# Optimization experiments

Hardware: AMD Instinct MI355X
Metric: run time of the kernel (lower is better)

The kernel has to match this reference:

```python
import jax, jax.numpy as jnp
import numpy as np

N = 50000      # total atoms/beads across batch
E = 800000     # total edges (avg degree 16)
H = 128        # hidden_channels
R = 50         # num_rbf
NB = 2         # n_interaction blocks
NG = 64        # num graphs in batch
NT = 100       # num atom types
CUT = 5.0      # upper distance cutoff


def setup_inputs() -> dict:
    key = jax.random.key(0)
    ks = jax.random.split(key, 20)
    atom_types = jax.random.randint(ks[0], (N,), 0, NT)
    pos = jax.random.uniform(ks[1], (N, 3), jnp.float32) * 30.0  # box of 30 Angstrom
    edge_index = jax.random.randint(ks[2], (2, E), 0, N)
    batch = jnp.sort(jax.random.randint(ks[3], (N,), 0, NG))

    def g(k, shape, fan_in):
        return jax.random.normal(k, shape, jnp.float32) * (1.0 / fan_in) ** 0.5

    emb = jax.random.normal(ks[4], (NT, H), jnp.float32) * 0.1
    # filter network per block: Linear(R->H) -> tanh -> Linear(H->H)
    fw1 = g(ks[5], (NB, R, H), R)
    fb1 = jnp.zeros((NB, H), jnp.float32)
    fw2 = g(ks[6], (NB, H, H), H)
    fb2 = jnp.zeros((NB, H), jnp.float32)
    # CFConv lin1 (no bias), lin2 (bias)
    lin1_w = g(ks[7], (NB, H, H), H)
    lin2_w = g(ks[8], (NB, H, H), H)
    lin2_b = jnp.zeros((NB, H), jnp.float32)
    # InteractionBlock output linear
    blk_w = g(ks[9], (NB, H, H), H)
    blk_b = jnp.zeros((NB, H), jnp.float32)
    # output network: Linear(H->H/2) -> tanh -> Linear(H/2->1)
    out_w1 = g(ks[10], (H, H // 2), H)
    out_b1 = jnp.zeros((H // 2,), jnp.float32)
    out_w2 = g(ks[11], (H // 2, 1), H // 2)
    out_b2 = jnp.zeros((1,), jnp.float32)
    return dict(atom_types=atom_types, pos=pos, edge_index=edge_index, batch=batch,
                emb=emb, fw1=fw1, fb1=fb1, fw2=fw2, fb2=fb2,
                lin1_w=lin1_w, lin2_w=lin2_w, lin2_b=lin2_b,
                blk_w=blk_w, blk_b=blk_b,
                out_w1=out_w1, out_b1=out_b1, out_w2=out_w2, out_b2=out_b2)


def reference(atom_types, pos, edge_index, batch, emb, fw1, fb1, fw2, fb2,
              lin1_w, lin2_w, lin2_b, blk_w, blk_b,
              out_w1, out_b1, out_w2, out_b2):
    src, dst = edge_index[0], edge_index[1]
    # pairwise distances along edges (eps keeps sqrt grad finite at coincident points)
    diff = pos[src] - pos[dst]                                  # [E,3]
    d = jnp.sqrt(jnp.sum(diff * diff, axis=-1) + 1e-12)         # [E]
    # Gaussian RBF expansion
    offsets = jnp.linspace(0.0, CUT, R)
    coeff = -0.5 / (offsets[1] - offsets[0]) ** 2
    rbf = jnp.exp(coeff * (d[:, None] - offsets) ** 2)          # [E,R]
    # cosine cutoff envelope
    Cenv = jnp.where(d < CUT, 0.5 * (jnp.cos(d * jnp.pi / CUT) + 1.0), 0.0)  # [E]

    x = emb[atom_types]                                          # [N,H]
    for i in range(NB):
        # filter generation from expanded distances
        W = jnp.tanh(rbf @ fw1[i] + fb1[i]) @ fw2[i] + fb2[i]    # [E,H]
        W = W * Cenv[:, None]
        # CFConv: lin1 -> gather*filter -> scatter-sum -> lin2
        h = x @ lin1_w[i]                                        # [N,H]
        msg = h[src] * W                                         # [E,H]
        agg = jax.ops.segment_sum(msg, dst, num_segments=N)      # [N,H]
        h = agg @ lin2_w[i] + lin2_b[i]
        # InteractionBlock: activation -> lin, residual add in SchNet.forward
        h = jnp.tanh(h)
        x = x + (h @ blk_w[i] + blk_b[i])
    # output network -> per-atom energy, scatter-sum per graph
    e = jnp.tanh(x @ out_w1 + out_b1) @ out_w2 + out_b2          # [N,1]
    energy = jax.ops.segment_sum(e, batch, num_segments=NG)      # [NG,1]
    return energy.flatten()
```

## Files before the change

kernel.cpp:

```cpp
#include <hip/hip_runtime.h>
#include <hip/hip_bf16.h>
#include <math.h>

#define H 128
#define RBF 50
#define CUTF 5.0f
#define PIF 3.14159265358979323846f
#define QT 1024
#define DEGC 16

__global__ __launch_bounds__(256) void prep_kernel(
    const float* __restrict__ pos, float4* __restrict__ pos4, int Nn,
    int4* __restrict__ zbase, int zquads,
    const float* __restrict__ fw1, const float* __restrict__ fb1,
    const float* __restrict__ fw2, const float* __restrict__ fb2,
    const float* __restrict__ lin1w, const float* __restrict__ lin2b,
    const float* __restrict__ blkw, const float* __restrict__ blkb,
    const float* __restrict__ emb,
    const float* __restrict__ ow1, const float* __restrict__ ob1,
    const float* __restrict__ ow2, const float* __restrict__ ob2,
    float* __restrict__ tab, float* __restrict__ e_type,
    float* __restrict__ htype0, float* __restrict__ htype1, int NT,
    int ZFB, int PB, int FB, int TB, int H0B)
{
// ... 105 lines not shown
        float x0 = emb[(size_t)ty * H + h0];
        float x1 = emb[(size_t)ty * H + h1];
        float a0 = 0.f, a1 = 0.f;
        #pragma unroll 8
        for (int k = 0; k < 64; ++k) {
            float bb2 = __shfl(x0, k, 64);
            a0 = fmaf(bb2, lin1w[k * H + h0], a0);
            a1 = fmaf(bb2, lin1w[k * H + h1], a1);
        }
        #pragma unroll 8
        for (int k = 0; k < 64; ++k) {
            float bb2 = __shfl(x1, k, 64);
            a0 = fmaf(bb2, lin1w[(64 + k) * H + h0], a0);
            a1 = fmaf(bb2, lin1w[(64 + k) * H + h1], a1);
        }
        htype0[(size_t)ty * H + h0] = a0;
        htype0[(size_t)ty * H + h1] = a1;
        return;
    }
    b -= H0B;
    {
        const int ty = b * 4 + (tid >> 6);
        if (ty >= NT) return;
        const float* bwp = blkw;
        float t0 = tanhf(lin2b[h0]);
        float t1 = tanhf(lin2b[h1]);
        float c0 = blkb[h0], c1 = blkb[h1];
        #pragma unroll 8
        for (int k = 0; k < 64; ++k) {
            float bb2 = __shfl(t0, k, 64);
            c0 = fmaf(bb2, bwp[k * H + h0], c0);
            c1 = fmaf(bb2, bwp[k * H + h1], c1);
        }
        #pragma unroll 8
        for (int k = 0; k < 64; ++k) {
            float bb2 = __shfl(t1, k, 64);
            c0 = fmaf(bb2, bwp[(64 + k) * H + h0], c0);
            c1 = fmaf(bb2, bwp[(64 + k) * H + h1], c1);
        }
        float x0 = emb[(size_t)ty * H + h0] + c0;
        float x1 = emb[(size_t)ty * H + h1] + c1;
        const float* l1 = lin1w + (size_t)H * H;
        float a0 = 0.f, a1 = 0.f;
        #pragma unroll 8
        for (int k = 0; k < 64; ++k) {
            float bb2 = __shfl(x0, k, 64);
            a0 = fmaf(bb2, l1[k * H + h0], a0);
            a1 = fmaf(bb2, l1[k * H + h1], a1);
        }
        #pragma unroll 8
        for (int k = 0; k < 64; ++k) {
            float bb2 = __shfl(x1, k, 64);
            a0 = fmaf(bb2, l1[(64 + k) * H + h0], a0);
            a1 = fmaf(bb2, l1[(64 + k) * H + h1], a1);
        }
        htype1[(size_t)ty * H + h0] = a0;
        htype1[(size_t)ty * H + h1] = a1;
    }
}

__global__ __launch_bounds__(256) void edge_prep_kernel(
    const float4* __restrict__ pos4, const int* __restrict__ ei, int E,
    int* __restrict__ deg, float* __restrict__ bdist, int* __restrict__ bsrc,
    int* __restrict__ is_src, int* __restrict__ is_dst)
{
    const int gtid = blockIdx.x * 256 + threadIdx.x;
    const int e0 = gtid * 4;

    int s[4], t[4];
    float d[4];
    bool act[4] = {false, false, false, false};

    if (e0 + 3 < E && (E & 3) == 0) {
        const int4 sv = *(const int4*)(ei + e0);
        const int4 tv = *(const int4*)(ei + E + e0);
        s[0] = sv.x; s[1] = sv.y; s[2] = sv.z; s[3] = sv.w;
        t[0] = tv.x; t[1] = tv.y; t[2] = tv.z; t[3] = tv.w;
        #pragma unroll
        for (int j = 0; j < 4; ++j) {
            float4 ps = pos4[s[j]], pt = pos4[t[j]];
            float dx = ps.x - pt.x, dy = ps.y - pt.y, dz = ps.z - pt.z;
            d[j] = sqrtf(dx * dx + dy * dy + dz * dz + 1e-12f);
            act[j] = (d[j] < CUTF);
        }
    } else if (e0 < E) {
        #pragma unroll
        for (int j = 0; j < 4; ++j) {
            int e = e0 + j;
            if (e < E) {
                s[j] = ei[e]; t[j] = ei[E + e];
                float4 ps = pos4[s[j]], pt = pos4[t[j]];
                float dx = ps.x - pt.x, dy = ps.y - pt.y, dz = ps.z - pt.z;
                d[j] = sqrtf(dx * dx + dy * dy + dz * dz + 1e-12f);
                act[j] = (d[j] < CUTF);
            }
        }
    }

    #pragma unroll
    for (int j = 0; j < 4; ++j) {
        if (act[j]) {
            is_src[s[j]] = 1;
            is_dst[t[j]] = 1;
            int k = atomicAdd(&deg[t[j]], 1);
            if (k < DEGC) {
                size_t bo = (size_t)t[j] * DEGC + k;
                bdist[bo] = d[j];
                bsrc[bo]  = s[j];
            }
        }
    }
}

__global__ __launch_bounds__(256) void compact_atoms_kernel(
    const int* __restrict__ is_src, const int* __restrict__ is_dst, int Nn,
    int* __restrict__ cnt4,
    int* __restrict__ dst_list, int* __restrict__ sd_list)
{
    __shared__ int wtot[2][4], wbase[2][4];
    const int tid = threadIdx.x;
    const int lane = tid & 63;
    const int wv = tid >> 6;
    int n = blockIdx.x * 256 + tid;
    bool v[2] = {false, false};
    if (n < Nn) {
        bool vd = is_dst[n] != 0;
        v[0] = vd;
        v[1] = vd && (is_src[n] != 0);
    }
    unsigned long long b[2];
    #pragma unroll
    for (int l = 0; l < 2; ++l) {
        b[l] = __ballot(v[l]);
        if (lane == 0) wtot[l][wv] = (int)__popcll(b[l]);
    }
    __syncthreads();
    if (tid == 0) {
        #pragma unroll
        for (int l = 0; l < 2; ++l) {
            int t0 = wtot[l][0], t1 = wtot[l][1], t2 = wtot[l][2], t3 = wtot[l][3];
            int tot = t0 + t1 + t2 + t3;
            int base = 0;
            if (tot) base = atomicAdd(cnt4 + 1 + l, tot);
            wbase[l][0] = base; wbase[l][1] = base + t0;
            wbase[l][2] = base + t0 + t1; wbase[l][3] = base + t0 + t1 + t2;
        }
    }
    __syncthreads();
    const unsigned long long ltm = ((unsigned long long)1 << lane) - 1;
    if (v[0]) dst_list[wbase[0][wv] + (int)__popcll(b[0] & ltm)] = n;
    if (v[1]) sd_list[wbase[1][wv] + (int)__popcll(b[1] & ltm)] = n;
}

#define STAGE_W(dstbuf, Wsrc, kcbase)                                        \
    {                                                                        \
        int wr = tid >> 5;                                                   \
        int wc = (tid & 31) * 4;                                             \
        _Pragma("unroll")                                                    \
        for (int p = 0; p < 4; ++p) {                                        \
            int row = wr + p * 8;                                            \
            *(float4*)&Ws[dstbuf][row][wc] =                                 \
                *(const float4*)((Wsrc) + (size_t)((kcbase) + row) * H + wc);\
        }                                                                    \
    }

__global__ __launch_bounds__(256) void update_x0_kernel(
    const float* __restrict__ bdist, const int* __restrict__ bsrc,
    const int* __restrict__ deg, const int* __restrict__ atype,
    const float* __restrict__ tab0, const float* __restrict__ htype0,
    const float* __restrict__ l2w, const float* __restrict__ l2b,
    const float* __restrict__ bw, const float* __restrict__ bb,
    const float* __restrict__ emb, const int* __restrict__ is_src,
    const float* __restrict__ l1w1,
    float* __restrict__ x, float* __restrict__ hbuf,
    const int* __restrict__ rows, const int* __restrict__ cntp)
{
    __shared__ float Ws[2][32][128];
    __shared__ float Tl[32][132];
    __shared__ int rlist[32], tlist[32], slist[32], dlist[32];

    const int tid = threadIdx.x;
    const int cnt = *cntp;
    const int r0 = (tid >> 4) * 2;
    const int c0 = (tid & 15) * 4;
    const float scale = (float)QT / CUTF;

    for (int tile = blockIdx.x; tile * 32 < cnt; tile += gridDim.x) {
        __syncthreads();
        if (tid < 32) {
            int idx = tile * 32 + tid;
            int r = (idx < cnt) ? rows[idx] : -1;
            rlist[tid] = r;
            tlist[tid] = (r >= 0) ? atype[r] : 0;
            slist[tid] = (r >= 0) ? is_src[r] : 0;
            int dn = (r >= 0) ? deg[r] : 0;
            dlist[tid] = dn < DEGC ? dn : DEGC;
        }
        __syncthreads();

        #pragma unroll
        for (int j = 0; j < 2; ++j) {
            float ag[8];
            #pragma unroll
            for (int c = 0; c < 8; ++c) ag[c] = 0.f;
            int r = rlist[r0 + j];
            int dn = dlist[r0 + j];
            for (int e = 0; e < dn; ++e) {
                size_t bo = (size_t)r * DEGC + e;
                float dd = bdist[bo];
                int s = bsrc[bo];
                int ty = atype[s];
                float p = dd * scale;
                int i0 = (int)p;
                if (i0 > QT - 1) i0 = QT - 1;
                float f = p - (float)i0;
                const float* tr = tab0 + (size_t)i0 * H;
                float4 ta = *(const float4*)(tr + c0);
                float4 tb = *(const float4*)(tr + H + c0);
                float4 tc = *(const float4*)(tr + c0 + 64);
                float4 td = *(const float4*)(tr + H + c0 + 64);
                const float* hr = htype0 + (size_t)ty * H;
                float4 ha = *(const float4*)(hr + c0);
                float4 hb = *(const float4*)(hr + c0 + 64);
                ag[0] = fmaf(fmaf(f, tb.x - ta.x, ta.x), ha.x, ag[0]);
                ag[1] = fmaf(fmaf(f, tb.y - ta.y, ta.y), ha.y, ag[1]);
                ag[2] = fmaf(fmaf(f, tb.z - ta.z, ta.z), ha.z, ag[2]);
                ag[3] = fmaf(fmaf(f, tb.w - ta.w, ta.w), ha.w, ag[3]);
                ag[4] = fmaf(fmaf(f, td.x - tc.x, tc.x), hb.x, ag[4]);
                ag[5] = fmaf(fmaf(f, td.y - tc.y, tc.y), hb.y, ag[5]);
                ag[6] = fmaf(fmaf(f, td.z - tc.z, tc.z), hb.z, ag[6]);
                ag[7] = fmaf(fmaf(f, td.w - tc.w, tc.w), hb.w, ag[7]);
            }
            *(float4*)&Tl[r0 + j][c0] = make_float4(ag[0], ag[1], ag[2], ag[3]);
            *(float4*)&Tl[r0 + j][c0 + 64] = make_float4(ag[4], ag[5], ag[6], ag[7]);
        }

        float acc[2][8];
        #pragma unroll
        for (int j = 0; j < 2; ++j)
            #pragma unroll
            for (int c = 0; c < 8; ++c) acc[j][c] = 0.f;

        STAGE_W(0, l2w, 0);
        __syncthreads();
        for (int kc = 0; kc < H; kc += 32) {
            int buf = (kc >> 5) & 1;
            if (kc + 32 < H) STAGE_W(buf ^ 1, l2w, kc + 32);
            #pragma unroll
            for (int k = 0; k < 32; k += 4) {
                float a_[2][4];
                #pragma unroll
                for (int j = 0; j < 2; ++j)
                    *(float4*)a_[j] = *(const float4*)&Tl[r0 + j][kc + k];
                #pragma unroll
                for (int kk = 0; kk < 4; ++kk) {
                    float4 wlo = *(const float4*)&Ws[buf][k + kk][c0];
                    float4 whi = *(const float4*)&Ws[buf][k + kk][c0 + 64];
                    float w_[8] = {wlo.x, wlo.y, wlo.z, wlo.w, whi.x, whi.y, whi.z, whi.w};
                    #pragma unroll
                    for (int j = 0; j < 2; ++j)
                        #pragma unroll
                        for (int c = 0; c < 8; ++c)
                            acc[j][c] = fmaf(a_[j][kk], w_[c], acc[j][c]);
                }
            }
            __syncthreads();
        }
        #pragma unroll
        for (int j = 0; j < 2; ++j) {
            float4 lo, hi;
            lo.x = tanhf(acc[j][0] + l2b[c0]);      lo.y = tanhf(acc[j][1] + l2b[c0 + 1]);
            lo.z = tanhf(acc[j][2] + l2b[c0 + 2]);  lo.w = tanhf(acc[j][3] + l2b[c0 + 3]);
            hi.x = tanhf(acc[j][4] + l2b[c0 + 64]); hi.y = tanhf(acc[j][5] + l2b[c0 + 65]);
            hi.z = tanhf(acc[j][6] + l2b[c0 + 66]); hi.w = tanhf(acc[j][7] + l2b[c0 + 67]);
            *(float4*)&Tl[r0 + j][c0] = lo;
            *(float4*)&Tl[r0 + j][c0 + 64] = hi;
        }

        float acc2[2][8];
        #pragma unroll
        for (int j = 0; j < 2; ++j)
            #pragma unroll
            for (int c = 0; c < 8; ++c) acc2[j][c] = 0.f;

        STAGE_W(0, bw, 0);
        __syncthreads();
        for (int kc = 0; kc < H; kc += 32) {
            int buf = (kc >> 5) & 1;
            if (kc + 32 < H) STAGE_W(buf ^ 1, bw, kc + 32);
            #pragma unroll
            for (int k = 0; k < 32; k += 4) {
                float a_[2][4];
                #pragma unroll
                for (int j = 0; j < 2; ++j)
                    *(float4*)a_[j] = *(const float4*)&Tl[r0 + j][kc + k];
                #pragma unroll
                for (int kk = 0; kk < 4; ++kk) {
                    float4 wlo = *(const float4*)&Ws[buf][k + kk][c0];
                    float4 whi = *(const float4*)&Ws[buf][k + kk][c0 + 64];
                    float w_[8] = {wlo.x, wlo.y, wlo.z, wlo.w, whi.x, whi.y, whi.z, whi.w};
                    #pragma unroll
                    for (int j = 0; j < 2; ++j)
                        #pragma unroll
                        for (int c = 0; c < 8; ++c)
                            acc2[j][c] = fmaf(a_[j][kk], w_[c], acc2[j][c]);
                }
            }
            __syncthreads();
        }
        #pragma unroll
        for (int j = 0; j < 2; ++j) {
            int r = rlist[r0 + j];
            int ty = tlist[r0 + j];
            #pragma unroll
            for (int hh = 0; hh < 2; ++hh) {
                int cb = c0 + hh * 64;
                float4 xv = make_float4(0.f, 0.f, 0.f, 0.f);
                if (r >= 0) xv = *(const float4*)(emb + (size_t)ty * H + cb);
                xv.x += acc2[j][hh * 4 + 0] + bb[cb];
                xv.y += acc2[j][hh * 4 + 1] + bb[cb + 1];
                xv.z += acc2[j][hh * 4 + 2] + bb[cb + 2];
                xv.w += acc2[j][hh * 4 + 3] + bb[cb + 3];
                *(float4*)&Tl[r0 + j][cb] = xv;
                if (r >= 0) *(float4*)(x + (size_t)r * H + cb) = xv;
            }
        }

        float acc3[2][8];
        #pragma unroll
        for (int j = 0; j < 2; ++j)
            #pragma unroll
            for (int c = 0; c < 8; ++c) acc3[j][c] = 0.f;

        STAGE_W(0, l1w1, 0);
        __syncthreads();
        for (int kc = 0; kc < H; kc += 32) {
            int buf = (kc >> 5) & 1;
            if (kc + 32 < H) STAGE_W(buf ^ 1, l1w1, kc + 32);
            #pragma unroll
            for (int k = 0; k < 32; k += 4) {
                float a_[2][4];
                #pragma unroll
                for (int j = 0; j < 2; ++j)
                    *(float4*)a_[j] = *(const float4*)&Tl[r0 + j][kc + k];
                #pragma unroll
                for (int kk = 0; kk < 4; ++kk) {
                    float4 wlo = *(const float4*)&Ws[buf][k + kk][c0];
                    float4 whi = *(const float4*)&Ws[buf][k + kk][c0 + 64];
                    float w_[8] = {wlo.x, wlo.y, wlo.z, wlo.w, whi.x, whi.y, whi.z, whi.w};
                    #pragma unroll
                    for (int j = 0; j < 2; ++j)
                        #pragma unroll
                        for (int c = 0; c < 8; ++c)
                            acc3[j][c] = fmaf(a_[j][kk], w_[c], acc3[j][c]);
                }
            }
            __syncthreads();
        }
        #pragma unroll
        for (int j = 0; j < 2; ++j) {
            int r = rlist[r0 + j];
            if (r < 0 || !slist[r0 + j]) continue;
            #pragma unroll
            for (int hh = 0; hh < 2; ++hh) {
                int cb = c0 + hh * 64;
                *(float4*)(hbuf + (size_t)r * H + cb) = make_float4(
                    acc3[j][hh * 4 + 0], acc3[j][hh * 4 + 1],
                    acc3[j][hh * 4 + 2], acc3[j][hh * 4 + 3]);
            }
        }
    }
}

__global__ __launch_bounds__(256) void update_e_kernel(
    const float* __restrict__ bdist, const int* __restrict__ bsrc,
    const int* __restrict__ deg, const int* __restrict__ atype,
    const int* __restrict__ is_dst,
    const float* __restrict__ tab1, const float* __restrict__ hbuf,
    const float* __restrict__ htype1,
    const float* __restrict__ l2w, const float* __restrict__ l2b,
    const float* __restrict__ bw, const float* __restrict__ bb,
    const float* __restrict__ x,
    const float* __restrict__ ow1, const float* __restrict__ ob1,
    const float* __restrict__ ow2, const float* __restrict__ ob2,
    float* __restrict__ e_atom,
    const int* __restrict__ rows, const int* __restrict__ cntp)
{
    __shared__ float Ws[2][32][128];
    __shared__ float Tl[32][132];
    __shared__ int rlist[32], dlist[32];

    const int tid = threadIdx.x;
    const int cnt = *cntp;
    const int r0 = (tid >> 4) * 2;
    const int c0 = (tid & 15) * 4;
    const float scale = (float)QT / CUTF;

    for (int tile = blockIdx.x; tile * 32 < cnt; tile += gridDim.x) {
        __syncthreads();
        if (tid < 32) {
            int idx = tile * 32 + tid;
            int r = (idx < cnt) ? rows[idx] : -1;
            rlist[tid] = r;
            int dn = (r >= 0) ? deg[r] : 0;
            dlist[tid] = dn < DEGC ? dn : DEGC;
        }
        __syncthreads();

        #pragma unroll
        for (int j = 0; j < 2; ++j) {
            float ag[8];
            #pragma unroll
            for (int c = 0; c < 8; ++c) ag[c] = 0.f;
            int r = rlist[r0 + j];
            int dn = dlist[r0 + j];
            for (int e = 0; e < dn; ++e) {
                size_t bo = (size_t)r * DEGC + e;
                float dd = bdist[bo];
                int s = bsrc[bo];
                float p = dd * scale;
                int i0 = (int)p;
                if (i0 > QT - 1) i0 = QT - 1;
                float f = p - (float)i0;
                const float* tr = tab1 + (size_t)i0 * H;
                float4 ta = *(const float4*)(tr + c0);
                float4 tb = *(const float4*)(tr + H + c0);
                float4 tc = *(const float4*)(tr + c0 + 64);
                float4 td = *(const float4*)(tr + H + c0 + 64);
                const float* hr = is_dst[s] ? (hbuf + (size_t)s * H)
                                            : (htype1 + (size_t)atype[s] * H);
                float4 ha = *(const float4*)(hr + c0);
                float4 hb = *(const float4*)(hr + c0 + 64);
                ag[0] = fmaf(fmaf(f, tb.x - ta.x, ta.x), ha.x, ag[0]);
                ag[1] = fmaf(fmaf(f, tb.y - ta.y, ta.y), ha.y, ag[1]);
                ag[2] = fmaf(fmaf(f, tb.z - ta.z, ta.z), ha.z, ag[2]);
                ag[3] = fmaf(fmaf(f, tb.w - ta.w, ta.w), ha.w, ag[3]);
                ag[4] = fmaf(fmaf(f, td.x - tc.x, tc.x), hb.x, ag[4]);
                ag[5] = fmaf(fmaf(f, td.y - tc.y, tc.y), hb.y, ag[5]);
                ag[6] = fmaf(fmaf(f, td.z - tc.z, tc.z), hb.z, ag[6]);
                ag[7] = fmaf(fmaf(f, td.w - tc.w, tc.w), hb.w, ag[7]);
            }
            *(float4*)&Tl[r0 + j][c0] = make_float4(ag[0], ag[1], ag[2], ag[3]);
            *(float4*)&Tl[r0 + j][c0 + 64] = make_float4(ag[4], ag[5], ag[6], ag[7]);
        }

        float acc[2][8];
        #pragma unroll
        for (int j = 0; j < 2; ++j)
            #pragma unroll
            for (int c = 0; c < 8; ++c) acc[j][c] = 0.f;

        STAGE_W(0, l2w, 0);
        __syncthreads();
        for (int kc = 0; kc < H; kc += 32) {
            int buf = (kc >> 5) & 1;
            if (kc + 32 < H) STAGE_W(buf ^ 1, l2w, kc + 32);
            #pragma unroll
            for (int k = 0; k < 32; k += 4) {
                float a_[2][4];
                #pragma unroll
                for (int j = 0; j < 2; ++j)
                    *(float4*)a_[j] = *(const float4*)&Tl[r0 + j][kc + k];
                #pragma unroll
                for (int kk = 0; kk < 4; ++kk) {
                    float4 wlo = *(const float4*)&Ws[buf][k + kk][c0];
                    float4 whi = *(const float4*)&Ws[buf][k + kk][c0 + 64];
                    float w_[8] = {wlo.x, wlo.y, wlo.z, wlo.w, whi.x, whi.y, whi.z, whi.w};
                    #pragma unroll
                    for (int j = 0; j < 2; ++j)
                        #pragma unroll
                        for (int c = 0; c < 8; ++c)
                            acc[j][c] = fmaf(a_[j][kk], w_[c], acc[j][c]);
                }
            }
            __syncthreads();
        }
        #pragma unroll
        for (int j = 0; j < 2; ++j) {
            float4 lo, hi;
            lo.x = tanhf(acc[j][0] + l2b[c0]);      lo.y = tanhf(acc[j][1] + l2b[c0 + 1]);
            lo.z = tanhf(acc[j][2] + l2b[c0 + 2]);  lo.w = tanhf(acc[j][3] + l2b[c0 + 3]);
            hi.x = tanhf(acc[j][4] + l2b[c0 + 64]); hi.y = tanhf(acc[j][5] + l2b[c0 + 65]);
            hi.z = tanhf(acc[j][6] + l2b[c0 + 66]); hi.w = tanhf(acc[j][7] + l2b[c0 + 67]);
            *(float4*)&Tl[r0 + j][c0] = lo;
            *(float4*)&Tl[r0 + j][c0 + 64] = hi;
        }

        float acc2[2][8];
        #pragma unroll
        for (int j = 0; j < 2; ++j)
            #pragma unroll
            for (int c = 0; c < 8; ++c) acc2[j][c] = 0.f;

        STAGE_W(0, bw, 0);
        __syncthreads();
        for (int kc = 0; kc < H; kc += 32) {
            int buf = (kc >> 5) & 1;
            if (kc + 32 < H) STAGE_W(buf ^ 1, bw, kc + 32);
            #pragma unroll
            for (int k = 0; k < 32; k += 4) {
                float a_[2][4];
                #pragma unroll
                for (int j = 0; j < 2; ++j)
                    *(float4*)a_[j] = *(const float4*)&Tl[r0 + j][kc + k];
                #pragma unroll
                for (int kk = 0; kk < 4; ++kk) {
                    float4 wlo = *(const float4*)&Ws[buf][k + kk][c0];
                    float4 whi = *(const float4*)&Ws[buf][k + kk][c0 + 64];
                    float w_[8] = {wlo.x, wlo.y, wlo.z, wlo.w, whi.x, whi.y, whi.z, whi.w};
                    #pragma unroll
                    for (int j = 0; j < 2; ++j)
                        #pragma unroll
                        for (int c = 0; c < 8; ++c)
                            acc2[j][c] = fmaf(a_[j][kk], w_[c], acc2[j][c]);
                }
            }
            __syncthreads();
        }
        #pragma unroll
        for (int j = 0; j < 2; ++j) {
            int r = rlist[r0 + j];
            #pragma unroll
            for (int hh = 0; hh < 2; ++hh) {
                int cb = c0 + hh * 64;
                float4 xv = make_float4(0.f, 0.f, 0.f, 0.f);
                if (r >= 0) xv = *(const float4*)(x + (size_t)r * H + cb);
                xv.x += acc2[j][hh * 4 + 0] + bb[cb];
                xv.y += acc2[j][hh * 4 + 1] + bb[cb + 1];
                xv.z += acc2[j][hh * 4 + 2] + bb[cb + 2];
                xv.w += acc2[j][hh * 4 + 3] + bb[cb + 3];
                *(float4*)&Tl[r0 + j][cb] = xv;
            }
        }

        float acc3[2][4];
        #pragma unroll
        for (int j = 0; j < 2; ++j)
            #pragma unroll
            for (int c = 0; c < 4; ++c) acc3[j][c] = 0.f;

        {
            int wr = tid >> 4;
            int wc = (tid & 15) * 4;
            #pragma unroll
            for (int p = 0; p < 2; ++p) {
                int row = wr + p * 16;
                *(float4*)&Ws[0][row][wc] = *(const float4*)(ow1 + (size_t)row * 64 + wc);
            }
        }
        __syncthreads();
        for (int kc = 0; kc < H; kc += 32) {
            int buf = (kc >> 5) & 1;
            if (kc + 32 < H) {
                int wr = tid >> 4;
                int wc = (tid & 15) * 4;
                #pragma unroll
                for (int p = 0; p < 2; ++p) {
                    int row = wr + p * 16;
                    *(float4*)&Ws[buf ^ 1][row][wc] =
                        *(const float4*)(ow1 + (size_t)(kc + 32 + row) * 64 + wc);
                }
            }
            #pragma unroll
            for (int k = 0; k < 32; ++k) {
                float a_[2];
                #pragma unroll
                for (int j = 0; j < 2; ++j) a_[j] = Tl[r0 + j][kc + k];
                float4 wv = *(const float4*)&Ws[buf][k][c0];
                #pragma unroll
                for (int j = 0; j < 2; ++j) {
                    acc3[j][0] = fmaf(a_[j], wv.x, acc3[j][0]);
                    acc3[j][1] = fmaf(a_[j], wv.y, acc3[j][1]);
                    acc3[j][2] = fmaf(a_[j], wv.z, acc3[j][2]);
                    acc3[j][3] = fmaf(a_[j], wv.w, acc3[j][3]);
                }
            }
            __syncthreads();
        }
        const float4 b1v = *(const float4*)(ob1 + c0);
        const float4 w2v = *(const float4*)(ow2 + c0);
        float ep[2];
        #pragma unroll
        for (int j = 0; j < 2; ++j) {
            float v0 = tanhf(acc3[j][0] + b1v.x);
            float v1 = tanhf(acc3[j][1] + b1v.y);
            float v2 = tanhf(acc3[j][2] + b1v.z);
            float v3 = tanhf(acc3[j][3] + b1v.w);
            ep[j] = v0 * w2v.x + v1 * w2v.y + v2 * w2v.z + v3 * w2v.w;
        }
        #pragma unroll
        for (int off = 1; off < 16; off <<= 1) {
            ep[0] += __shfl_xor(ep[0], off, 64);
            ep[1] += __shfl_xor(ep[1], off, 64);
        }
        if ((tid & 15) == 0) {
            const float b2v = ob2[0];
            #pragma unroll
            for (int j = 0; j < 2; ++j) {
                int r = rlist[r0 + j];
                if (r >= 0) e_atom[r] = ep[j] + b2v;
            }
        }
    }
}

__global__ __launch_bounds__(256) void energy_graph_kernel(
    const int* __restrict__ batch, const int* __restrict__ atype,
    const int* __restrict__ is_dst, const float* __restrict__ e_atom,
    const float* __restrict__ e_type, float* __restrict__ energy, int Nn)
{
    const int g = blockIdx.x;
    int lo = 0, hi = Nn;
    while (lo < hi) { int m = (lo + hi) >> 1; if (batch[m] < g) lo = m + 1; else hi = m; }
    const int start = lo;
    hi = Nn;
    while (lo < hi) { int m = (lo + hi) >> 1; if (batch[m] < g + 1) lo = m + 1; else hi = m; }
    const int end = lo;

    float s = 0.0f;
    for (int n = start + (int)threadIdx.x; n < end; n += 256)
        s += is_dst[n] ? e_atom[n] : e_type[atype[n]];
    #pragma unroll
    for (int off = 32; off; off >>= 1) s += __shfl_xor(s, off, 64);
    __shared__ float wp[4];
    if ((threadIdx.x & 63) == 0) wp[threadIdx.x >> 6] = s;
    __syncthreads();
    if (threadIdx.x == 0) energy[g] = wp[0] + wp[1] + wp[2] + wp[3];
}

extern "C" void kernel_launch(void* const* d_in, const int* in_sizes, int n_in,
                              void* d_out, int out_size, void* d_ws, size_t ws_size,
                              hipStream_t stream)
{
    const int*   atype = (const int*)  d_in[0];
    const float* pos   = (const float*)d_in[1];
    const int*   ei    = (const int*)  d_in[2];
    const int*   batch = (const int*)  d_in[3];
    const float* emb   = (const float*)d_in[4];
    const float* fw1   = (const float*)d_in[5];
    const float* fb1   = (const float*)d_in[6];
    const float* fw2   = (const float*)d_in[7];
    const float* fb2   = (const float*)d_in[8];
    const float* lin1w = (const float*)d_in[9];
    const float* lin2w = (const float*)d_in[10];
    const float* lin2b = (const float*)d_in[11];
    const float* blkw  = (const float*)d_in[12];
    const float* blkb  = (const float*)d_in[13];
    const float* ow1   = (const float*)d_in[14];
    const float* ob1   = (const float*)d_in[15];
    const float* ow2   = (const float*)d_in[16];
    const float* ob2   = (const float*)d_in[17];

    const int Nn = in_sizes[0];
    const int E  = in_sizes[2] / 2;
    const int NT = in_sizes[4] / H;
    float* energy = (float*)d_out;

    char* w = (char*)d_ws;
    int*   cnt  = (int*)w;
    int*   is_src = cnt + 32;
    int*   is_dst = is_src + Nn;
    int*   deg    = is_dst + Nn;
    float* x    = (float*)(deg + Nn);
    float* hbuf = x + (size_t)Nn * H;
    float* bdist = hbuf + (size_t)Nn * H;
    int*   bsrc  = (int*)(bdist + (size_t)Nn * DEGC);
    int*   dst_list = bsrc + (size_t)Nn * DEGC;
    int*   sd_list  = dst_list + Nn;
    float* tab  = (float*)(sd_list + Nn);
    float* e_type = tab + 2 * (size_t)(QT + 1) * H;
    float* htype0 = e_type + 128;
    float* htype1 = htype0 + (size_t)NT * H;
    float* e_atom = htype1 + (size_t)NT * H;
    float4* pos4 = (float4*)(e_atom + Nn);

    const size_t zbytes = 128 + 3 * (size_t)Nn * 4;
    const int zquads = (int)((zbytes + 15) / 16);
    const int ZFB = (zquads + 255) / 256;
    const int PB  = (Nn + 255) / 256;
    const int FB  = (2 * (QT + 1) + 3) / 4;
    const int TB  = (NT + 3) / 4;
    const int H0B = (NT + 3) / 4;
    const int H1B = (NT + 3) / 4;

    prep_kernel<<<ZFB + PB + FB + TB + H0B + H1B, 256, 0, stream>>>(
        pos, pos4, Nn, (int4*)cnt, zquads,
        fw1, fb1, fw2, fb2, lin1w, lin2b, blkw, blkb, emb,
        ow1, ob1, ow2, ob2, tab, e_type, htype0, htype1, NT,
        ZFB, PB, FB, TB, H0B);

    edge_prep_kernel<<<(E + 1023) / 1024, 256, 0, stream>>>(
        pos4, ei, E, deg, bdist, bsrc, is_src, is_dst);

    compact_atoms_kernel<<<(Nn + 255) / 256, 256, 0, stream>>>(
        is_src, is_dst, Nn, cnt, dst_list, sd_list);

    update_x0_kernel<<<512, 256, 0, stream>>>(
        bdist, bsrc, deg, atype, tab, htype0,
        lin2w, lin2b, blkw, blkb, emb, is_src, lin1w + (size_t)H * H,
        x, hbuf, dst_list, cnt + 1);

    update_e_kernel<<<512, 256, 0, stream>>>(
        bdist, bsrc, deg, atype, is_dst,
        tab + (size_t)(QT + 1) * H, hbuf, htype1,
        lin2w + (size_t)H * H, lin2b + H, blkw + (size_t)H * H, blkb + H,
        x, ow1, ob1, ow2, ob2, e_atom, dst_list, cnt + 1);

    energy_graph_kernel<<<out_size, 256, 0, stream>>>(
        batch, atype, is_dst, e_atom, e_type, energy, Nn);
}
```

Before: 202.9 us.

## Split fused interaction kernels into wave-per-row gather and column-split GEMM kernels

Result: slower. 218.3 us (+7.6%).

```diff
diff --git a/kernel.cpp b/kernel.cpp
--- a/kernel.cpp
+++ b/kernel.cpp
@@ -281,440 +281,218 @@
     if (v[1]) sd_list[wbase[1][wv] + (int)__popcll(b[1] & ltm)] = n;
 }
 
-#define STAGE_W(dstbuf, Wsrc, kcbase)                                        \
-    {                                                                        \
-        int wr = tid >> 5;                                                   \
-        int wc = (tid & 31) * 4;                                             \
-        _Pragma("unroll")                                                    \
-        for (int p = 0; p < 4; ++p) {                                        \
-            int row = wr + p * 8;                                            \
-            *(float4*)&Ws[dstbuf][row][wc] =                                 \
-                *(const float4*)((Wsrc) + (size_t)((kcbase) + row) * H + wc);\
-        }                                                                    \
-    }
-
-__global__ __launch_bounds__(256) void update_x0_kernel(
+__global__ __launch_bounds__(256) void gather_kernel(
     const float* __restrict__ bdist, const int* __restrict__ bsrc,
     const int* __restrict__ deg, const int* __restrict__ atype,
-    const float* __restrict__ tab0, const float* __restrict__ htype0,
-    const float* __restrict__ l2w, const float* __restrict__ l2b,
-    const float* __restrict__ bw, const float* __restrict__ bb,
-    const float* __restrict__ emb, const int* __restrict__ is_src,
-    const float* __restrict__ l1w1,
-    float* __restrict__ x, float* __restrict__ hbuf,
-    const int* __restrict__ rows, const int* __restrict__ cntp)
-{
-    __shared__ float Ws[2][32][128];
-    __shared__ float Tl[32][132];
-    __shared__ int rlist[32], tlist[32], slist[32], dlist[32];
+    const float* __restrict__ tab, const float* __restrict__ hbuf,
+    const float* __restrict__ htype, const int* __restrict__ is_dst,
+    float* __restrict__ agg,
+    const int* __restrict__ rows, const int* __restrict__ cntp, int pass1)
+{
+    const int tid = threadIdx.x;
+    const int lane = tid & 63;
+    const int wid = (blockIdx.x * 256 + tid) >> 6;
+    const int nw  = (gridDim.x * 256) >> 6;
+    const int cnt = *cntp;
+    const float scale = (float)QT / CUTF;
+
+    for (int i = wid; i < cnt; i += nw) {
+        int r = rows[i];
+        int dn = deg[r];
+        if (dn > DEGC) dn = DEGC;
+        float a0 = 0.f, a1 = 0.f;
+        for (int e = 0; e < dn; ++e) {
+            size_t bo = (size_t)r * DEGC + e;
+            float dd = bdist[bo];
+            int s = bsrc[bo];
+            float p = dd * scale;
+            int i0 = (int)p;
+            if (i0 > QT - 1) i0 = QT - 1;
+            float f = p - (float)i0;
+            const float* tr = tab + (size_t)i0 * H;
+            float wl = fmaf(f, tr[H + lane] - tr[lane], tr[lane]);
+            float wh = fmaf(f, tr[H + 64 + lane] - tr[64 + lane], tr[64 + lane]);
+            const float* hr = (pass1 && is_dst[s]) ? (hbuf + (size_t)s * H)
+                                                   : (htype + (size_t)atype[s] * H);
+            a0 = fmaf(wl, hr[lane], a0);
+            a1 = fmaf(wh, hr[64 + lane], a1);
+        }
+        agg[(size_t)r * H + lane] = a0;
+        agg[(size_t)r * H + 64 + lane] = a1;
+    }
+}
+
+__global__ __launch_bounds__(256) void gemm_cols_kernel(
+    const float* __restrict__ IN, const float* __restrict__ W,
+    const float* __restrict__ bias, float* __restrict__ OUT,
+    const int* __restrict__ rows, const int* __restrict__ cntp,
+    const int* __restrict__ atype, const float* __restrict__ emb,
+    const float* __restrict__ residp, const int* __restrict__ pred,
+    int act_tanh)
+{
+    __shared__ float As[32][36];
+    __shared__ float Ws[32][68];
+    __shared__ int rlist[32], tylist[32], plist[32];
 
     const int tid = threadIdx.x;
     const int cnt = *cntp;
     const int r0 = (tid >> 4) * 2;
     const int c0 = (tid & 15) * 4;
-    const float scale = (float)QT / CUTF;
-
-    for (int tile = blockIdx.x; tile * 32 < cnt; tile += gridDim.x) {
+
+    for (int b2 = blockIdx.x; (b2 >> 1) * 32 < cnt; b2 += gridDim.x) {
+        const int tile = b2 >> 1;
+        const int ch = (b2 & 1) * 64;
         __syncthreads();
         if (tid < 32) {
             int idx = tile * 32 + tid;
             int r = (idx < cnt) ? rows[idx] : -1;
             rlist[tid] = r;
-            tlist[tid] = (r >= 0) ? atype[r] : 0;
-            slist[tid] = (r >= 0) ? is_src[r] : 0;
-            int dn = (r >= 0) ? deg[r] : 0;
-            dlist[tid] = dn < DEGC ? dn : DEGC;
+            tylist[tid] = (atype && r >= 0) ? atype[r] : 0;
+            plist[tid] = pred ? ((r >= 0) ? pred[r] : 0) : 1;
         }
         __syncthreads();
 
-        #pragma unroll
-        for (int j = 0; j < 2; ++j) {
-            float ag[8];
-            #pragma unroll
-            for (int c = 0; c < 8; ++c) ag[c] = 0.f;
-            int r = rlist[r0 + j];
-            int dn = dlist[r0 + j];
-            for (int e = 0; e < dn; ++e) {
-                size_t bo = (size_t)r * DEGC + e;
-                float dd = bdist[bo];
-                int s = bsrc[bo];
-                int ty = atype[s];
-                float p = dd * scale;
-                int i0 = (int)p;
-                if (i0 > QT - 1) i0 = QT - 1;
-                float f = p - (float)i0;
-                const float* tr = tab0 + (size_t)i0 * H;
-                float4 ta = *(const float4*)(tr + c0);
-                float4 tb = *(const float4*)(tr + H + c0);
-                float4 tc = *(const float4*)(tr + c0 + 64);
-                float4 td = *(const float4*)(tr + H + c0 + 64);
-                const float* hr = htype0 + (size_t)ty * H;
-                float4 ha = *(const float4*)(hr + c0);
-                float4 hb = *(const float4*)(hr + c0 + 64);
-                ag[0] = fmaf(fmaf(f, tb.x - ta.x, ta.x), ha.x, ag[0]);
-                ag[1] = fmaf(fmaf(f, tb.y - ta.y, ta.y), ha.y, ag[1]);
-                ag[2] = fmaf(fmaf(f, tb.z - ta.z, ta.z), ha.z, ag[2]);
-                ag[3] = fmaf(fmaf(f, tb.w - ta.w, ta.w), ha.w, ag[3]);
-                ag[4] = fmaf(fmaf(f, td.x - tc.x, tc.x), hb.x, ag[4]);
-                ag[5] = fmaf(fmaf(f, td.y - tc.y, tc.y), hb.y, ag[5]);
-                ag[6] = fmaf(fmaf(f, td.z - tc.z, tc.z), hb.z, ag[6]);
-                ag[7] = fmaf(fmaf(f, td.w - tc.w, tc.w), hb.w, ag[7]);
-            }
-            *(float4*)&Tl[r0 + j][c0] = make_float4(ag[0], ag[1], ag[2], ag[3]);
-            *(float4*)&Tl[r0 + j][c0 + 64] = make_float4(ag[4], ag[5], ag[6], ag[7]);
-        }
-
-        float acc[2][8];
+        float acc[2][4];
         #pragma unroll
         for (int j = 0; j < 2; ++j)
             #pragma unroll
-            for (int c = 0; c < 8; ++c) acc[j][c] = 0.f;
-
-        STAGE_W(0, l2w, 0);
-        __syncthreads();
+            for (int c = 0; c < 4; ++c) acc[j][c] = 0.f;
+
         for (int kc = 0; kc < H; kc += 32) {
-            int buf = (kc >> 5) & 1;
-            if (kc + 32 < H) STAGE_W(buf ^ 1, l2w, kc + 32);
+            {
+                int lr = tid >> 3;
+                int kk = (tid & 7) * 4;
+                int r = rlist[lr];
+                float4 v = make_float4(0.f, 0.f, 0.f, 0.f);
+                if (r >= 0) v = *(const float4*)(IN + (size_t)r * H + kc + kk);
+                *(float4*)&As[lr][kk] = v;
+            }
+            {
+                #pragma unroll
+                for (int p = 0; p < 2; ++p) {
+                    int lin = tid + p * 256;
+                    int row = lin >> 4;
+                    int wc = (lin & 15) * 4;
+                    *(float4*)&Ws[row][wc] =
+                        *(const float4*)(W + (size_t)(kc + row) * H + ch + wc);
+                }
+            }
+            __syncthreads();
             #pragma unroll
-            for (int k = 0; k < 32; k += 4) {
-                float a_[2][4];
-                #pragma unroll
-                for (int j = 0; j < 2; ++j)
-                    *(float4*)a_[j] = *(const float4*)&Tl[r0 + j][kc + k];
-                #pragma unroll
-                for (int kk = 0; kk < 4; ++kk) {
-                    float4 wlo = *(const float4*)&Ws[buf][k + kk][c0];
-                    float4 whi = *(const float4*)&Ws[buf][k + kk][c0 + 64];
-                    float w_[8] = {wlo.x, wlo.y, wlo.z, wlo.w, whi.x, whi.y, whi.z, whi.w};
-                    #pragma unroll
-                    for (int j = 0; j < 2; ++j)
-                        #pragma unroll
-                        for (int c = 0; c < 8; ++c)
-                            acc[j][c] = fmaf(a_[j][kk], w_[c], acc[j][c]);
-                }
+            for (int k = 0; k < 32; ++k) {
+                float a0 = As[r0][k], a1 = As[r0 + 1][k];
+                float4 wv = *(const float4*)&Ws[k][c0];
+                acc[0][0] = fmaf(a0, wv.x, acc[0][0]);
+                acc[0][1] = fmaf(a0, wv.y, acc[0][1]);
+                acc[0][2] = fmaf(a0, wv.z, acc[0][2]);
+                acc[0][3] = fmaf(a0, wv.w, acc[0][3]);
+                acc[1][0] = fmaf(a1, wv.x, acc[1][0]);
+                acc[1][1] = fmaf(a1, wv.y, acc[1][1]);
+                acc[1][2] = fmaf(a1, wv.z, acc[1][2]);
+                acc[1][3] = fmaf(a1, wv.w, acc[1][3]);
             }
             __syncthreads();
         }
-        #pragma unroll
-        for (int j = 0; j < 2; ++j) {
-            float4 lo, hi;
-            lo.x = tanhf(acc[j][0] + l2b[c0]);      lo.y = tanhf(acc[j][1] + l2b[c0 + 1]);
-            lo.z = tanhf(acc[j][2] + l2b[c0 + 2]);  lo.w = tanhf(acc[j][3] + l2b[c0 + 3]);
-            hi.x = tanhf(acc[j][4] + l2b[c0 + 64]); hi.y = tanhf(acc[j][5] + l2b[c0 + 65]);
-            hi.z = tanhf(acc[j][6] + l2b[c0 + 66]); hi.w = tanhf(acc[j][7] + l2b[c0 + 67]);
-            *(float4*)&Tl[r0 + j][c0] = lo;
-            *(float4*)&Tl[r0 + j][c0 + 64] = hi;
-        }
-
-        float acc2[2][8];
-        #pragma unroll
-        for (int j = 0; j < 2; ++j)
-            #pragma unroll
-            for (int c = 0; c < 8; ++c) acc2[j][c] = 0.f;
-
-        STAGE_W(0, bw, 0);
-        __syncthreads();
-        for (int kc = 0; kc < H; kc += 32) {
-            int buf = (kc >> 5) & 1;
-            if (kc + 32 < H) STAGE_W(buf ^ 1, bw, kc + 32);
-            #pragma unroll
-            for (int k = 0; k < 32; k += 4) {
-                float a_[2][4];
-                #pragma unroll
-                for (int j = 0; j < 2; ++j)
-                    *(float4*)a_[j] = *(const float4*)&Tl[r0 + j][kc + k];
-                #pragma unroll
-                for (int kk = 0; kk < 4; ++kk) {
-                    float4 wlo = *(const float4*)&Ws[buf][k + kk][c0];
-                    float4 whi = *(const float4*)&Ws[buf][k + kk][c0 + 64];
-                    float w_[8] = {wlo.x, wlo.y, wlo.z, wlo.w, whi.x, whi.y, whi.z, whi.w};
-                    #pragma unroll
-                    for (int j = 0; j < 2; ++j)
-                        #pragma unroll
-                        for (int c = 0; c < 8; ++c)
-                            acc2[j][c] = fmaf(a_[j][kk], w_[c], acc2[j][c]);
-                }
-            }
-            __syncthreads();
-        }
+
         #pragma unroll
         for (int j = 0; j < 2; ++j) {
             int r = rlist[r0 + j];
-            int ty = tlist[r0 + j];
-            #pragma unroll
-            for (int hh = 0; hh < 2; ++hh) {
-                int cb = c0 + hh * 64;
-                float4 xv = make_float4(0.f, 0.f, 0.f, 0.f);
-                if (r >= 0) xv = *(const float4*)(emb + (size_t)ty * H + cb);
-                xv.x += acc2[j][hh * 4 + 0] + bb[cb];
-                xv.y += acc2[j][hh * 4 + 1] + bb[cb + 1];
-                xv.z += acc2[j][hh * 4 + 2] + bb[cb + 2];
-                xv.w += acc2[j][hh * 4 + 3] + bb[cb + 3];
-                *(float4*)&Tl[r0 + j][cb] = xv;
-                if (r >= 0) *(float4*)(x + (size_t)r * H + cb) = xv;
-            }
-        }
-
-        float acc3[2][8];
-        #pragma unroll
-        for (int j = 0; j < 2; ++j)
-            #pragma unroll
-            for (int c = 0; c < 8; ++c) acc3[j][c] = 0.f;
-
-        STAGE_W(0, l1w1, 0);
-        __syncthreads();
-        for (int kc = 0; kc < H; kc += 32) {
-            int buf = (kc >> 5) & 1;
-            if (kc + 32 < H) STAGE_W(buf ^ 1, l1w1, kc + 32);
-            #pragma unroll
-            for (int k = 0; k < 32; k += 4) {
-                float a_[2][4];
-                #pragma unroll
-                for (int j = 0; j < 2; ++j)
-                    *(float4*)a_[j] = *(const float4*)&Tl[r0 + j][kc + k];
-                #pragma unroll
-                for (int kk = 0; kk < 4; ++kk) {
-                    float4 wlo = *(const float4*)&Ws[buf][k + kk][c0];
-                    float4 whi = *(const float4*)&Ws[buf][k + kk][c0 + 64];
-                    float w_[8] = {wlo.x, wlo.y, wlo.z, wlo.w, whi.x, whi.y, whi.z, whi.w};
-                    #pragma unroll
-                    for (int j = 0; j < 2; ++j)
-                        #pragma unroll
-                        for (int c = 0; c < 8; ++c)
-                            acc3[j][c] = fmaf(a_[j][kk], w_[c], acc3[j][c]);
-                }
-            }
-            __syncthreads();
-        }
-        #pragma unroll
-        for (int j = 0; j < 2; ++j) {
-            int r = rlist[r0 + j];
-            if (r < 0 || !slist[r0 + j]) continue;
-            #pragma unroll
-            for (int hh = 0; hh < 2; ++hh) {
-                int cb = c0 + hh * 64;
-                *(float4*)(hbuf + (size_t)r * H + cb) = make_float4(
-                    acc3[j][hh * 4 + 0], acc3[j][hh * 4 + 1],
-                    acc3[j][hh * 4 + 2], acc3[j][hh * 4 + 3]);
-            }
-        }
-    }
-}
-
-__global__ __launch_bounds__(256) void update_e_kernel(
-    const float* __restrict__ bdist, const int* __restrict__ bsrc,
-    const int* __restrict__ deg, const int* __restrict__ atype,
-    const int* __restrict__ is_dst,
-    const float* __restrict__ tab1, const float* __restrict__ hbuf,
-    const float* __restrict__ htype1,
-    const float* __restrict__ l2w, const float* __restrict__ l2b,
-    const float* __restrict__ bw, const float* __restrict__ bb,
-    const float* __restrict__ x,
-    const float* __restrict__ ow1, const float* __restrict__ ob1,
-    const float* __restrict__ ow2, const float* __restrict__ ob2,
-    float* __restrict__ e_atom,
+            if (r < 0 || !plist[r0 + j]) continue;
+            float v0 = acc[j][0], v1 = acc[j][1], v2 = acc[j][2], v3 = acc[j][3];
+            if (bias) {
+                v0 += bias[ch + c0];     v1 += bias[ch + c0 + 1];
+                v2 += bias[ch + c0 + 2]; v3 += bias[ch + c0 + 3];
+            }
+            if (act_tanh) {
+                v0 = tanhf(v0); v1 = tanhf(v1); v2 = tanhf(v2); v3 = tanhf(v3);
+            }
+            if (emb) {
+                float4 ev = *(const float4*)(emb + (size_t)tylist[r0 + j] * H + ch + c0);
+                v0 += ev.x; v1 += ev.y; v2 += ev.z; v3 += ev.w;
+            }
+            if (residp) {
+                float4 rv = *(const float4*)(residp + (size_t)r * H + ch + c0);
+                v0 += rv.x; v1 += rv.y; v2 += rv.z; v3 += rv.w;
+            }
+            *(float4*)(OUT + (size_t)r * H + ch + c0) = make_float4(v0, v1, v2, v3);
+        }
+    }
+}
+
+__global__ __launch_bounds__(256) void head_kernel(
+    const float* __restrict__ XF, const float* __restrict__ ow1,
+    const float* __restrict__ ob1, const float* __restrict__ ow2,
+    const float* __restrict__ ob2, float* __restrict__ e_atom,
     const int* __restrict__ rows, const int* __restrict__ cntp)
 {
-    __shared__ float Ws[2][32][128];
-    __shared__ float Tl[32][132];
-    __shared__ int rlist[32], dlist[32];
+    __shared__ float Xs[32][36];
+    __shared__ float Ws[32][68];
+    __shared__ int rlist[32];
 
     const int tid = threadIdx.x;
     const int cnt = *cntp;
     const int r0 = (tid >> 4) * 2;
     const int c0 = (tid & 15) * 4;
-    const float scale = (float)QT / CUTF;
 
     for (int tile = blockIdx.x; tile * 32 < cnt; tile += gridDim.x) {
         __syncthreads();
         if (tid < 32) {
             int idx = tile * 32 + tid;
-            int r = (idx < cnt) ? rows[idx] : -1;
-            rlist[tid] = r;
-            int dn = (r >= 0) ? deg[r] : 0;
-            dlist[tid] = dn < DEGC ? dn : DEGC;
+            rlist[tid] = (idx < cnt) ? rows[idx] : -1;
         }
         __syncthreads();
 
-        #pragma unroll
-        for (int j = 0; j < 2; ++j) {
-            float ag[8];
-            #pragma unroll
-            for (int c = 0; c < 8; ++c) ag[c] = 0.f;
-            int r = rlist[r0 + j];
-            int dn = dlist[r0 + j];
-            for (int e = 0; e < dn; ++e) {
-                size_t bo = (size_t)r * DEGC + e;
-                float dd = bdist[bo];
-                int s = bsrc[bo];
-                float p = dd * scale;
-                int i0 = (int)p;
-                if (i0 > QT - 1) i0 = QT - 1;
-                float f = p - (float)i0;
-                const float* tr = tab1 + (size_t)i0 * H;
-                float4 ta = *(const float4*)(tr + c0);
-                float4 tb = *(const float4*)(tr + H + c0);
-                float4 tc = *(const float4*)(tr + c0 + 64);
-                float4 td = *(const float4*)(tr + H + c0 + 64);
-                const float* hr = is_dst[s] ? (hbuf + (size_t)s * H)
-                                            : (htype1 + (size_t)atype[s] * H);
-                float4 ha = *(const float4*)(hr + c0);
-                float4 hb = *(const float4*)(hr + c0 + 64);
-                ag[0] = fmaf(fmaf(f, tb.x - ta.x, ta.x), ha.x, ag[0]);
-                ag[1] = fmaf(fmaf(f, tb.y - ta.y, ta.y), ha.y, ag[1]);
-                ag[2] = fmaf(fmaf(f, tb.z - ta.z, ta.z), ha.z, ag[2]);
-                ag[3] = fmaf(fmaf(f, tb.w - ta.w, ta.w), ha.w, ag[3]);
-                ag[4] = fmaf(fmaf(f, td.x - tc.x, tc.x), hb.x, ag[4]);
-                ag[5] = fmaf(fmaf(f, td.y - tc.y, tc.y), hb.y, ag[5]);
-                ag[6] = fmaf(fmaf(f, td.z - tc.z, tc.z), hb.z, ag[6]);
-                ag[7] = fmaf(fmaf(f, td.w - tc.w, tc.w), hb.w, ag[7]);
-            }
-            *(float4*)&Tl[r0 + j][c0] = make_float4(ag[0], ag[1], ag[2], ag[3]);
-            *(float4*)&Tl[r0 + j][c0 + 64] = make_float4(ag[4], ag[5], ag[6], ag[7]);
-        }
-
-        float acc[2][8];
+        float acc[2][4];
         #pragma unroll
         for (int j = 0; j < 2; ++j)
             #pragma unroll
-            for (int c = 0; c < 8; ++c) acc[j][c] = 0.f;
-
-        STAGE_W(0, l2w, 0);
-        __syncthreads();
+            for (int c = 0; c < 4; ++c) acc[j][c] = 0.f;
+
         for (int kc = 0; kc < H; kc += 32) {
-            int buf = (kc >> 5) & 1;
-            if (kc + 32 < H) STAGE_W(buf ^ 1, l2w, kc + 32);
-            #pragma unroll
-            for (int k = 0; k < 32; k += 4) {
-                float a_[2][4];
-                #pragma unroll
-                for (int j = 0; j < 2; ++j)
-                    *(float4*)a_[j] = *(const float4*)&Tl[r0 + j][kc + k];
-                #pragma unroll
-                for (int kk = 0; kk < 4; ++kk) {
-                    float4 wlo = *(const float4*)&Ws[buf][k + kk][c0];
-                    float4 whi = *(const float4*)&Ws[buf][k + kk][c0 + 64];
-                    float w_[8] = {wlo.x, wlo.y, wlo.z, wlo.w, whi.x, whi.y, whi.z, whi.w};
-                    #pragma unroll
-                    for (int j = 0; j < 2; ++j)
-                        #pragma unroll
-                        for (int c = 0; c < 8; ++c)
-                            acc[j][c] = fmaf(a_[j][kk], w_[c], acc[j][c]);
-                }
-            }
-            __syncthreads();
-        }
-        #pragma unroll
-        for (int j = 0; j < 2; ++j) {
-            float4 lo, hi;
-            lo.x = tanhf(acc[j][0] + l2b[c0]);      lo.y = tanhf(acc[j][1] + l2b[c0 + 1]);
-            lo.z = tanhf(acc[j][2] + l2b[c0 + 2]);  lo.w = tanhf(acc[j][3] + l2b[c0 + 3]);
-            hi.x = tanhf(acc[j][4] + l2b[c0 + 64]); hi.y = tanhf(acc[j][5] + l2b[c0 + 65]);
-            hi.z = tanhf(acc[j][6] + l2b[c0 + 66]); hi.w = tanhf(acc[j][7] + l2b[c0 + 67]);
-            *(float4*)&Tl[r0 + j][c0] = lo;
-            *(float4*)&Tl[r0 + j][c0 + 64] = hi;
-        }
-
-        float acc2[2][8];
-        #pragma unroll
-        for (int j = 0; j < 2; ++j)
-            #pragma unroll
-            for (int c = 0; c < 8; ++c) acc2[j][c] = 0.f;
-
-        STAGE_W(0, bw, 0);
-        __syncthreads();
-        for (int kc = 0; kc < H; kc += 32) {
-            int buf = (kc >> 5) & 1;
-            if (kc + 32 < H) STAGE_W(buf ^ 1, bw, kc + 32);
-            #pragma unroll
-            for (int k = 0; k < 32; k += 4) {
-                float a_[2][4];
-                #pragma unroll
-                for (int j = 0; j < 2; ++j)
-                    *(float4*)a_[j] = *(const float4*)&Tl[r0 + j][kc + k];
-                #pragma unroll
-                for (int kk = 0; kk < 4; ++kk) {
-                    float4 wlo = *(const float4*)&Ws[buf][k + kk][c0];
-                    float4 whi = *(const float4*)&Ws[buf][k + kk][c0 + 64];
-                    float w_[8] = {wlo.x, wlo.y, wlo.z, wlo.w, whi.x, whi.y, whi.z, whi.w};
-                    #pragma unroll
-                    for (int j = 0; j < 2; ++j)
-                        #pragma unroll
-                        for (int c = 0; c < 8; ++c)
-                            acc2[j][c] = fmaf(a_[j][kk], w_[c], acc2[j][c]);
-                }
-            }
-            __syncthreads();
-        }
-        #pragma unroll
-        for (int j = 0; j < 2; ++j) {
-            int r = rlist[r0 + j];
-            #pragma unroll
-            for (int hh = 0; hh < 2; ++hh) {
-                int cb = c0 + hh * 64;
-                float4 xv = make_float4(0.f, 0.f, 0.f, 0.f);
-                if (r >= 0) xv = *(const float4*)(x + (size_t)r * H + cb);
-                xv.x += acc2[j][hh * 4 + 0] + bb[cb];
-                xv.y += acc2[j][hh * 4 + 1] + bb[cb + 1];
-                xv.z += acc2[j][hh * 4 + 2] + bb[cb + 2];
-                xv.w += acc2[j][hh * 4 + 3] + bb[cb + 3];
-                *(float4*)&Tl[r0 + j][cb] = xv;
-            }
-        }
-
-        float acc3[2][4];
-        #pragma unroll
-        for (int j = 0; j < 2; ++j)
-            #pragma unroll
-            for (int c = 0; c < 4; ++c) acc3[j][c] = 0.f;
-
-        {
-            int wr = tid >> 4;
-            int wc = (tid & 15) * 4;
-            #pragma unroll
-            for (int p = 0; p < 2; ++p) {
-                int row = wr + p * 16;
-                *(float4*)&Ws[0][row][wc] = *(const float4*)(ow1 + (size_t)row * 64 + wc);
-            }
-        }
-        __syncthreads();
-        for (int kc = 0; kc < H; kc += 32) {
-            int buf = (kc >> 5) & 1;
-            if (kc + 32 < H) {
-                int wr = tid >> 4;
-                int wc = (tid & 15) * 4;
+            {
+                int lr = tid >> 3;
+                int kk = (tid & 7) * 4;
+                int r = rlist[lr];
+                float4 v = make_float4(0.f, 0.f, 0.f, 0.f);
+                if (r >= 0) v = *(const float4*)(XF + (size_t)r * H + kc + kk);
+                *(float4*)&Xs[lr][kk] = v;
+            }
+            {
                 #pragma unroll
                 for (int p = 0; p < 2; ++p) {
-                    int row = wr + p * 16;
-                    *(float4*)&Ws[buf ^ 1][row][wc] =
-                        *(const float4*)(ow1 + (size_t)(kc + 32 + row) * 64 + wc);
+                    int lin = tid + p * 256;
+                    int row = lin >> 4;
+                    int wc = (lin & 15) * 4;
+                    *(float4*)&Ws[row][wc] =
+                        *(const float4*)(ow1 + (size_t)(kc + row) * 64 + wc);
                 }
             }
+            __syncthreads();
             #pragma unroll
             for (int k = 0; k < 32; ++k) {
-                float a_[2];
-                #pragma unroll
-                for (int j = 0; j < 2; ++j) a_[j] = Tl[r0 + j][kc + k];
-                float4 wv = *(const float4*)&Ws[buf][k][c0];
-                #pragma unroll
-                for (int j = 0; j < 2; ++j) {
-                    acc3[j][0] = fmaf(a_[j], wv.x, acc3[j][0]);
-                    acc3[j][1] = fmaf(a_[j], wv.y, acc3[j][1]);
-                    acc3[j][2] = fmaf(a_[j], wv.z, acc3[j][2]);
-                    acc3[j][3] = fmaf(a_[j], wv.w, acc3[j][3]);
-                }
+                float a0 = Xs[r0][k], a1 = Xs[r0 + 1][k];
+                float4 wv = *(const float4*)&Ws[k][c0];
+                acc[0][0] = fmaf(a0, wv.x, acc[0][0]);
+                acc[0][1] = fmaf(a0, wv.y, acc[0][1]);
+                acc[0][2] = fmaf(a0, wv.z, acc[0][2]);
+                acc[0][3] = fmaf(a0, wv.w, acc[0][3]);
+                acc[1][0] = fmaf(a1, wv.x, acc[1][0]);
+                acc[1][1] = fmaf(a1, wv.y, acc[1][1]);
+                acc[1][2] = fmaf(a1, wv.z, acc[1][2]);
+                acc[1][3] = fmaf(a1, wv.w, acc[1][3]);
             }
             __syncthreads();
         }
+
         const float4 b1v = *(const float4*)(ob1 + c0);
         const float4 w2v = *(const float4*)(ow2 + c0);
         float ep[2];
         #pragma unroll
         for (int j = 0; j < 2; ++j) {
-            float v0 = tanhf(acc3[j][0] + b1v.x);
-            float v1 = tanhf(acc3[j][1] + b1v.y);
-            float v2 = tanhf(acc3[j][2] + b1v.z);
-            float v3 = tanhf(acc3[j][3] + b1v.w);
+            float v0 = tanhf(acc[j][0] + b1v.x);
+            float v1 = tanhf(acc[j][1] + b1v.y);
+            float v2 = tanhf(acc[j][2] + b1v.z);
+            float v3 = tanhf(acc[j][3] + b1v.w);
             ep[j] = v0 * w2v.x + v1 * w2v.y + v2 * w2v.z + v3 * w2v.w;
         }
         #pragma unroll
@@ -792,7 +570,10 @@
     int*   deg    = is_dst + Nn;
     float* x    = (float*)(deg + Nn);
     float* hbuf = x + (size_t)Nn * H;
-    float* bdist = hbuf + (size_t)Nn * H;
+    float* agg  = hbuf + (size_t)Nn * H;
+    float* tbuf = agg + (size_t)Nn * H;
+    float* xf   = tbuf + (size_t)Nn * H;
+    float* bdist = xf + (size_t)Nn * H;
     int*   bsrc  = (int*)(bdist + (size_t)Nn * DEGC);
     int*   dst_list = bsrc + (size_t)Nn * DEGC;
     int*   sd_list  = dst_list + Nn;
@@ -824,16 +605,36 @@
     compact_atoms_kernel<<<(Nn + 255) / 256, 256, 0, stream>>>(
         is_src, is_dst, Nn, cnt, dst_list, sd_list);
 
-    update_x0_kernel<<<512, 256, 0, stream>>>(
-        bdist, bsrc, deg, atype, tab, htype0,
-        lin2w, lin2b, blkw, blkb, emb, is_src, lin1w + (size_t)H * H,
-        x, hbuf, dst_list, cnt + 1);
-
-    update_e_kernel<<<512, 256, 0, stream>>>(
-        bdist, bsrc, deg, atype, is_dst,
-        tab + (size_t)(QT + 1) * H, hbuf, htype1,
-        lin2w + (size_t)H * H, lin2b + H, blkw + (size_t)H * H, blkb + H,
-        x, ow1, ob1, ow2, ob2, e_atom, dst_list, cnt + 1);
+    const float* l1w1 = lin1w + (size_t)H * H;
+    const float* l2w0 = lin2w;
+    const float* l2w1 = lin2w + (size_t)H * H;
+    const float* bw0  = blkw;
+    const float* bw1  = blkw + (size_t)H * H;
+
+    gather_kernel<<<2048, 256, 0, stream>>>(
+        bdist, bsrc, deg, atype, tab, nullptr, htype0, is_dst,
+        agg, dst_list, cnt + 1, 0);
+    gemm_cols_kernel<<<1024, 256, 0, stream>>>(
+        agg, l2w0, lin2b, tbuf, dst_list, cnt + 1,
+        nullptr, nullptr, nullptr, nullptr, 1);
+    gemm_cols_kernel<<<1024, 256, 0, stream>>>(
+        tbuf, bw0, blkb, x, dst_list, cnt + 1,
+        atype, emb, nullptr, nullptr, 0);
+    gemm_cols_kernel<<<1024, 256, 0, stream>>>(
+        x, l1w1, nullptr, hbuf, dst_list, cnt + 1,
+        nullptr, nullptr, nullptr, is_src, 0);
+
+    gather_kernel<<<2048, 256, 0, stream>>>(
+        bdist, bsrc, deg, atype, tab + (size_t)(QT + 1) * H, hbuf, htype1, is_dst,
+        agg, dst_list, cnt + 1, 1);
+    gemm_cols_kernel<<<1024, 256, 0, stream>>>(
+        agg, l2w1, lin2b + H, tbuf, dst_list, cnt + 1,
+        nullptr, nullptr, nullptr, nullptr, 1);
+    gemm_cols_kernel<<<1024, 256, 0, stream>>>(
+        tbuf, bw1, blkb + H, xf, dst_list, cnt + 1,
+        nullptr, nullptr, x, nullptr, 0);
+    head_kernel<<<512, 256, 0, stream>>>(
+        xf, ow1, ob1, ow2, ob2, e_atom, dst_list, cnt + 1);
 
     energy_graph_kernel<<<out_size, 256, 0, stream>>>(
         batch, atype, is_dst, e_atom, e_type, energy, Nn);
```
